# Performance work log

Hardware: AMD Instinct MI355X
Metric: run time of the kernel (lower is better)

The kernel has to match this reference:

```python
import jax, jax.numpy as jnp
import numpy as np

H = 12          # heads
DH = 64         # head dim
BS = 64         # BigBird block size
R = 3           # random blocks per query block per head
SCALE = 1.0 / np.sqrt(DH)
EPS = 1e-12     # BERT-style LayerNorm eps
NEG = -1e9


def _plan(n_blocks, seed=0):
    """Deterministic BigBird block plan: per (head, middle query block) the
    attended key-block indices [global0, win-1, win0, win+1, globalN-1, R randoms]
    plus a validity mask that kills duplicate blocks (first occurrence wins)."""
    rng = np.random.RandomState(seed)
    c = 5 + R
    idx = np.zeros((H, n_blocks - 2, c), np.int32)
    for h in range(H):
        for i in range(1, n_blocks - 1):
            base = [0, i - 1, i, i + 1, n_blocks - 1]
            cand = [j for j in range(1, n_blocks - 1) if j not in set(base)]
            idx[h, i - 1, :5] = base
            idx[h, i - 1, 5:] = rng.choice(cand, size=R, replace=False)
    valid = np.ones(idx.shape, bool)
    for a in range(c):
        for b in range(a):
            valid[..., a] &= idx[..., a] != idx[..., b]
    return jnp.asarray(idx), jnp.asarray(valid)


def _ln(x, g, b):
    mu = jnp.mean(x, -1, keepdims=True)
    v = jnp.mean(jnp.square(x - mu), -1, keepdims=True)
    return (x - mu) * jax.lax.rsqrt(v + EPS) * g + b


def _attn(h, wq, bq, wk, bk, wv, bv, idx, valid, am):
    B, S, D = h.shape
    n = S // BS
    c = idx.shape[-1]

    def heads(W, b):
        return (h @ W + b).reshape(B, S, H, DH).transpose(0, 2, 1, 3)  # [B,H,S,dh]

    q, k, v = heads(wq, bq), heads(wk, bk), heads(wv, bv)
    qb = q.reshape(B, H, n, BS, DH)
    kb = k.reshape(B, H, n, BS, DH)
    vb = v.reshape(B, H, n, BS, DH)

    # --- global query blocks (first & last): dense attention over all keys ---
    qg = jnp.concatenate([qb[:, :, 0], qb[:, :, -1]], axis=2)          # [B,H,2*BS,dh]
    sg = jnp.einsum('bhqd,bhkd->bhqk', qg, k) * SCALE
    sg = jnp.where(am[:, None, None, :] > 0, sg, NEG)
    og = jnp.einsum('bhqk,bhkd->bhqd', jax.nn.softmax(sg, -1), v)

    # --- middle query blocks: gather window+global+random key blocks ---
    hh = jnp.arange(H)[:, None, None]
    kg = kb[:, hh, idx]                                                # [B,H,n-2,c,BS,dh]
    vg = vb[:, hh, idx]
    s = jnp.einsum('bhiqd,bhickd->bhiqck', qb[:, :, 1:-1], kg) * SCALE # [B,H,n-2,BS,c,BS]
    amb = am.reshape(B, n, BS)
    amg = amb[:, idx]                                                  # [B,H,n-2,c,BS]
    mask = valid[None, :, :, None, :, None] & (amg[:, :, :, None, :, :] > 0)
    s = jnp.where(mask, s, NEG)
    p = jax.nn.softmax(s.reshape(B, H, n - 2, BS, c * BS), -1).reshape(s.shape)
    om = jnp.einsum('bhiqck,bhickd->bhiqd', p, vg)                     # [B,H,n-2,BS,dh]

    o = jnp.concatenate([og[:, :, None, :BS], om, og[:, :, None, BS:]], axis=2)
    return o.reshape(B, H, S, DH).transpose(0, 2, 1, 3).reshape(B, S, D)


def reference(x, attention_mask, Wp, bp, pos_emb, tok_emb, ln_emb_g, ln_emb_b,
              Wq, bq, Wk, bk, Wv, bv, Wo, bo, ln1_g, ln1_b,
              W1, b1f, W2, b2f, ln2_g, ln2_b, Wc1, bc1, Wc2, bc2):
    B, S, _ = x.shape
    idx, valid = _plan(S // BS)
    am = attention_mask
    h = x @ Wp + bp + pos_emb[:S][None] + tok_emb[None, None]
    h = _ln(h, ln_emb_g, ln_emb_b)

    def layer(hc, p):
        wq, bq_, wk, bk_, wv, bv_, wo, bo_, g1, be1, w1, bf1, w2, bf2, g2, be2 = p
        a = _attn(hc, wq, bq_, wk, bk_, wv, bv_, idx, valid, am) @ wo + bo_
        hc = _ln(hc + a, g1, be1)
        f = jax.nn.gelu(hc @ w1 + bf1, approximate=True) @ w2 + bf2
        hc = _ln(hc + f, g2, be2)
        return hc, None

    h, _ = jax.lax.scan(layer, h, (Wq, bq, Wk, bk, Wv, bv, Wo, bo, ln1_g, ln1_b,
                                   W1, b1f, W2, b2f, ln2_g, ln2_b))
    cls = h[:, 0]
    return jax.nn.relu(cls @ Wc1 + bc1) @ Wc2 + bc2


def setup_inputs() -> dict:
    B, S, IN, D, FF, L, OUT = 1, 4096, 1280, 768, 3072, 12, 2000
    key = jax.random.key(0)
    ks = iter(jax.random.split(key, 32))
    rn = lambda sh, s=0.02: jax.random.normal(next(ks), sh, jnp.float32) * s
    return {
        'x': jax.random.normal(next(ks), (B, S, IN), jnp.float32),
        'attention_mask': jnp.ones((B, S), jnp.int32),
        'Wp': rn((IN, D)), 'bp': jnp.zeros((D,), jnp.float32),
        'pos_emb': rn((S, D)), 'tok_emb': rn((D,)),
        'ln_emb_g': jnp.ones((D,), jnp.float32), 'ln_emb_b': jnp.zeros((D,), jnp.float32),
        'Wq': rn((L, D, D)), 'bq': jnp.zeros((L, D), jnp.float32),
        'Wk': rn((L, D, D)), 'bk': jnp.zeros((L, D), jnp.float32),
        'Wv': rn((L, D, D)), 'bv': jnp.zeros((L, D), jnp.float32),
        'Wo': rn((L, D, D)), 'bo': jnp.zeros((L, D), jnp.float32),
        'ln1_g': jnp.ones((L, D), jnp.float32), 'ln1_b': jnp.zeros((L, D), jnp.float32),
        'W1': rn((L, D, FF)), 'b1f': jnp.zeros((L, FF), jnp.float32),
        'W2': rn((L, FF, D)), 'b2f': jnp.zeros((L, D), jnp.float32),
        'ln2_g': jnp.ones((L, D), jnp.float32), 'ln2_b': jnp.zeros((L, D), jnp.float32),
        'Wc1': rn((D, 512)), 'bc1': jnp.zeros((512,), jnp.float32),
        'Wc2': rn((512, OUT)), 'bc2': jnp.zeros((OUT,), jnp.float32),
    }
```

## Files before the change

kernel.cpp:

```cpp
#include <hip/hip_runtime.h>
#include <cstdint>
#include <cstring>

typedef unsigned short u16;
typedef uint32_t u32;
typedef __attribute__((ext_vector_type(8))) short s16x8;
typedef float f32x4 __attribute__((ext_vector_type(4)));
typedef uint32_t u32x4 __attribute__((ext_vector_type(4)));

#define ATTN_SCALE 0.125f
#define NEGV -1e9f
#define GNSPLIT 16

__device__ inline float bf2f(u16 u) { return __uint_as_float(((u32)u) << 16); }
__device__ inline u16 f2bf(float f) {
    u32 x = __float_as_uint(f);
    u32 r = (x + 0x7fffu + ((x >> 16) & 1u)) >> 16;
    return (u16)r;
}
__device__ inline float rdf(const void* p, size_t i, int fl) {
    return fl ? ((const float*)p)[i] : bf2f(((const u16*)p)[i]);
}
__device__ inline float gelu_f(float x) {
    float t = 0.7978845608028654f * (x + 0.044715f * x * x * x);
    return 0.5f * x * (1.0f + tanhf(t));
}
__device__ inline f32x4 zero4() { f32x4 z = {0.f, 0.f, 0.f, 0.f}; return z; }

__global__ void sniff_k(const void* x, int* flag) {
    const u16* p = (const u16*)x;
    const int tid = threadIdx.x;
    int wild = 0;
    for (int i = tid; i < 2048; i += 64) {
        const u16 v = p[i];
        const int e = (v >> 7) & 0xff;
        if (v != 0 && (e >= 0x8f || e <= 0x5f)) wild++;
    }
#pragma unroll
    for (int m = 32; m; m >>= 1) wild += __shfl_xor(wild, m, 64);
    if (tid == 0) *flag = (wild > 64) ? 1 : 0;
}

__global__ void sentinel_k(float* out, float v, int n) {
    const int i = blockIdx.x * 256 + threadIdx.x;
    if (i < n) out[i] = v;
}

__global__ __launch_bounds__(256) void cast_k(const void* src, u16* dst, int n, const int* flag) {
    const int fl = *flag;
    const int i = blockIdx.x * 256 + threadIdx.x;
    if (i < n) dst[i] = fl ? f2bf(((const float*)src)[i]) : ((const u16*)src)[i];
}

#define LDK 72

__global__ __launch_bounds__(256) void gemm_bf16(
    const u16* __restrict__ A, const u16* __restrict__ BT,
    const void* __restrict__ bias, u16* __restrict__ C,
    int M, int N, int K, int act, const int* __restrict__ flag)
{
    __shared__ alignas(16) u16 Alds[128 * LDK];
    __shared__ alignas(16) u16 Blds[128 * LDK];
    const int fl = *flag;
    const int tid = threadIdx.x;
    const int w = tid >> 6, lane = tid & 63;
    const int quad = lane >> 4, l16 = lane & 15;
    const int wm = (w >> 1) * 64, wn = (w & 1) * 64;
    const int m0 = blockIdx.y * 128, n0 = blockIdx.x * 128;

    f32x4 acc[4][4];
    const f32x4 zv = {0.f, 0.f, 0.f, 0.f};
#pragma unroll
    for (int i = 0; i < 4; i++)
#pragma unroll
        for (int j = 0; j < 4; j++) acc[i][j] = zv;

    const int srow = tid >> 3;
    const int scol = (tid & 7) * 8;

    for (int k0 = 0; k0 < K; k0 += 64) {
        __syncthreads();
#pragma unroll
        for (int it = 0; it < 4; ++it) {
            const int row = srow + it * 32;
            *(u32x4*)(Alds + row * LDK + scol) =
                *(const u32x4*)(A + (size_t)(m0 + row) * K + k0 + scol);
            *(u32x4*)(Blds + row * LDK + scol) =
                *(const u32x4*)(BT + (size_t)(n0 + row) * K + k0 + scol);
        }
        __syncthreads();
#pragma unroll
        for (int kk = 0; kk < 2; ++kk) {
            s16x8 af[4], bfr[4];
#pragma unroll
            for (int i = 0; i < 4; i++) {
                u32x4 t_ = *(const u32x4*)(Alds + (wm + i * 16 + l16) * LDK + kk * 32 + quad * 8);
                af[i] = __builtin_bit_cast(s16x8, t_);
            }
#pragma unroll
            for (int j = 0; j < 4; j++) {
                u32x4 t_ = *(const u32x4*)(Blds + (wn + j * 16 + l16) * LDK + kk * 32 + quad * 8);
                bfr[j] = __builtin_bit_cast(s16x8, t_);
            }
#pragma unroll
            for (int i = 0; i < 4; i++)
#pragma unroll
                for (int j = 0; j < 4; j++)
                    acc[i][j] = __builtin_amdgcn_mfma_f32_16x16x32_bf16(af[i], bfr[j], acc[i][j], 0, 0, 0);
        }
    }
#pragma unroll
    for (int j = 0; j < 4; j++) {
        const int col = n0 + wn + j * 16 + l16;
        const float bv = rdf(bias, col, fl);
#pragma unroll
        for (int i = 0; i < 4; i++) {
            const int row = m0 + wm + i * 16 + quad * 4;
#pragma unroll
            for (int r = 0; r < 4; r++) {
                float xv = acc[i][j][r] + bv;
                if (act) xv = gelu_f(xv);
                C[(size_t)(row + r) * N + col] = f2bf(xv);
            }
        }
    }
}

__global__ __launch_bounds__(256) void transpose_k(
    const void* __restrict__ src, u16* __restrict__ dst, int R, int C,
    const int* __restrict__ flag)
{
    __shared__ float tile[32][33];
    const int fl = *flag;
    const int tx = threadIdx.x & 31, ty = threadIdx.x >> 5;
    const int bx = blockIdx.x, by = blockIdx.y;
#pragma unroll
    for (int rr = 0; rr < 32; rr += 8)
        tile[ty + rr][tx] = rdf(src, (size_t)(by * 32 + ty + rr) * C + bx * 32 + tx, fl);
    __syncthreads();
#pragma unroll
    for (int rr = 0; rr < 32; rr += 8)
        dst[(size_t)(bx * 32 + ty + rr) * R + by * 32 + tx] = f2bf(tile[tx][ty + rr]);
}

__global__ __launch_bounds__(256) void ln_k(
    const float* hin, const u16* __restrict__ delta,
    const void* __restrict__ pos, const void* __restrict__ tok,
    const void* __restrict__ g, const void* __restrict__ b,
    float* hout, u16* __restrict__ hbf, int mode, const int* __restrict__ flag)
{
    __shared__ float red[4];
    const int fl = *flag;
    const int s = blockIdx.x, tid = threadIdx.x;
    const size_t base = (size_t)s * 768;
    float x0 = bf2f(delta[base + tid]);
    float x1 = bf2f(delta[base + tid + 256]);
    float x2 = bf2f(delta[base + tid + 512]);
    if (mode == 0) {
        x0 += hin[base + tid]; x1 += hin[base + tid + 256]; x2 += hin[base + tid + 512];
    } else {
        x0 += rdf(pos, base + tid, fl) + rdf(tok, tid, fl);
        x1 += rdf(pos, base + tid + 256, fl) + rdf(tok, tid + 256, fl);
        x2 += rdf(pos, base + tid + 512, fl) + rdf(tok, tid + 512, fl);
    }
    float sm = x0 + x1 + x2;
#pragma unroll
    for (int m = 32; m; m >>= 1) sm += __shfl_xor(sm, m, 64);
    if ((tid & 63) == 0) red[tid >> 6] = sm;
    __syncthreads();
    const float mu = (red[0] + red[1] + red[2] + red[3]) * (1.0f / 768.0f);
    __syncthreads();
    const float d0 = x0 - mu, d1 = x1 - mu, d2 = x2 - mu;
    float vs = d0 * d0 + d1 * d1 + d2 * d2;
#pragma unroll
    for (int m = 32; m; m >>= 1) vs += __shfl_xor(vs, m, 64);
    if ((tid & 63) == 0) red[tid >> 6] = vs;
    __syncthreads();
    const float inv = rsqrtf((red[0] + red[1] + red[2] + red[3]) * (1.0f / 768.0f) + 1e-12f);
    const float y0 = d0 * inv * rdf(g, tid, fl) + rdf(b, tid, fl);
    const float y1 = d1 * inv * rdf(g, tid + 256, fl) + rdf(b, tid + 256, fl);
    const float y2 = d2 * inv * rdf(g, tid + 512, fl) + rdf(b, tid + 512, fl);
    hout[base + tid] = y0; hout[base + tid + 256] = y1; hout[base + tid + 512] = y2;
    hbf[base + tid] = f2bf(y0); hbf[base + tid + 256] = f2bf(y1); hbf[base + tid + 512] = f2bf(y2);
}

__global__ __launch_bounds__(256) void attn_mid(
    const u16* __restrict__ q, const u16* __restrict__ k, const u16* __restrict__ v,
    const int* __restrict__ am, const unsigned char* __restrict__ plan,
    u16* __restrict__ ctx)
{
    __shared__ alignas(16) u16 vt[64 * 72];
    __shared__ alignas(16) u16 plw[4][16 * 72];
    const int bid = blockIdx.x;
    const int h = bid / 62;
    const int i = 1 + (bid - h * 62);
    const int tid = threadIdx.x;
    const int w = tid >> 6, lane = tid & 63;
    const int quad = lane >> 4, l16 = lane & 15;
    const int rowbase = i * 64 + w * 16;

    const unsigned long long pw = *(const unsigned long long*)(plan + (size_t)(h * 62 + (i - 1)) * 8);

    s16x8 qa[2];
#pragma unroll
    for (int kk = 0; kk < 2; kk++) {
        u32x4 t_ = *(const u32x4*)(q + (size_t)(rowbase + l16) * 768 + h * 64 + kk * 32 + quad * 8);
        qa[kk] = __builtin_bit_cast(s16x8, t_);
    }

    f32x4 o[4];
    float mrow[4], lrow[4];
#pragma unroll
    for (int j = 0; j < 4; j++) o[j] = zero4();
#pragma unroll
    for (int r = 0; r < 4; r++) { mrow[r] = NEGV; lrow[r] = 0.f; }

    for (int t = 0; t < 8; t++) {
        const int pv = (int)((pw >> (8 * t)) & 0xff);
        const int kb = pv & 63;
        const int blkok = !(pv & 64);

        __syncthreads();
        {
            const int kr = tid & 63;
            const int seg = tid >> 6;
            const u16* vp = v + (size_t)(kb * 64 + kr) * 768 + h * 64 + seg * 16;
#pragma unroll
            for (int hc = 0; hc < 2; hc++) {
                u32x4 t_ = *(const u32x4*)(vp + hc * 8);
                const u16* e = (const u16*)&t_;
#pragma unroll
                for (int j = 0; j < 8; j++)
                    vt[(seg * 16 + hc * 8 + j) * 72 + kr] = e[j];
            }
        }

        f32x4 st[4];
#pragma unroll
        for (int jt = 0; jt < 4; jt++) {
            st[jt] = zero4();
            const u16* kp = k + (size_t)(kb * 64 + jt * 16 + l16) * 768 + h * 64 + quad * 8;
#pragma unroll
            for (int kk = 0; kk < 2; kk++) {
                u32x4 t_ = *(const u32x4*)(kp + kk * 32);
                s16x8 bf_ = __builtin_bit_cast(s16x8, t_);
                st[jt] = __builtin_amdgcn_mfma_f32_16x16x32_bf16(qa[kk], bf_, st[jt], 0, 0, 0);
            }
        }
#pragma unroll
        for (int jt = 0; jt < 4; jt++) {
            const int key = kb * 64 + jt * 16 + l16;
            const bool ok = blkok && (am[key] > 0);
#pragma unroll
            for (int r = 0; r < 4; r++)
                st[jt][r] = ok ? st[jt][r] * ATTN_SCALE : NEGV;
        }
        float mt[4];
#pragma unroll
        for (int r = 0; r < 4; r++)
            mt[r] = fmaxf(fmaxf(st[0][r], st[1][r]), fmaxf(st[2][r], st[3][r]));
#pragma unroll
        for (int m_ = 1; m_ < 16; m_ <<= 1) {
#pragma unroll
            for (int r = 0; r < 4; r++)
                mt[r] = fmaxf(mt[r], __shfl_xor(mt[r], m_, 64));
        }
        float sc[4], ps[4];
#pragma unroll
        for (int r = 0; r < 4; r++) {
            const float mn = fmaxf(mrow[r], mt[r]);
            sc[r] = __expf(mrow[r] - mn);
            mrow[r] = mn;
            ps[r] = 0.f;
        }
#pragma unroll
        for (int jt = 0; jt < 4; jt++) {
#pragma unroll
            for (int r = 0; r < 4; r++) {
                const float p = __expf(st[jt][r] - mrow[r]);
                st[jt][r] = p;
                ps[r] += p;
            }
        }
#pragma unroll
        for (int m_ = 1; m_ < 16; m_ <<= 1) {
#pragma unroll
            for (int r = 0; r < 4; r++)
                ps[r] += __shfl_xor(ps[r], m_, 64);
        }
#pragma unroll
        for (int r = 0; r < 4; r++) lrow[r] = lrow[r] * sc[r] + ps[r];

        u16* pb = &plw[w][0];
#pragma unroll
        for (int jt = 0; jt < 4; jt++) {
#pragma unroll
            for (int r = 0; r < 4; r++)
                pb[(quad * 4 + r) * 72 + jt * 16 + l16] = f2bf(st[jt][r]);
        }
#pragma unroll
        for (int j = 0; j < 4; j++) {
#pragma unroll
            for (int r = 0; r < 4; r++)
                o[j][r] *= sc[r];
        }
        __syncthreads();

#pragma unroll
        for (int kk = 0; kk < 2; kk++) {
            s16x8 pa;
            {
                u32x4 t_ = *(const u32x4*)(pb + l16 * 72 + kk * 32 + quad * 8);
                pa = __builtin_bit_cast(s16x8, t_);
            }
#pragma unroll
            for (int jt2 = 0; jt2 < 4; jt2++) {
                u32x4 t_ = *(const u32x4*)(vt + (jt2 * 16 + l16) * 72 + kk * 32 + quad * 8);
                s16x8 vb = __builtin_bit_cast(s16x8, t_);
                o[jt2] = __builtin_amdgcn_mfma_f32_16x16x32_bf16(pa, vb, o[jt2], 0, 0, 0);
            }
        }
    }

    float invl[4];
#pragma unroll
    for (int r = 0; r < 4; r++) invl[r] = 1.0f / lrow[r];
#pragma unroll
    for (int jt2 = 0; jt2 < 4; jt2++) {
#pragma unroll
        for (int r = 0; r < 4; r++)
            ctx[(size_t)(rowbase + quad * 4 + r) * 768 + h * 64 + jt2 * 16 + l16] =
                f2bf(o[jt2][r] * invl[r]);
    }
}

__global__ __launch_bounds__(256) void attn_global_mfma(
    const u16* __restrict__ q, const u16* __restrict__ k, const u16* __restrict__ v,
    const int* __restrict__ am, float* __restrict__ po, float* __restrict__ pml)
{
    __shared__ alignas(16) u16 vt[64 * 72];
    __shared__ alignas(16) u16 plw[4][16 * 72];
    const int bid = blockIdx.x;
    const int h = bid / (2 * GNSPLIT);
    const int rem = bid - h * 2 * GNSPLIT;
    const int qb = rem / GNSPLIT;
    const int sp = rem - qb * GNSPLIT;
    const int tid = threadIdx.x;
    const int w = tid >> 6, lane = tid & 63;
    const int quad = lane >> 4, l16 = lane & 15;
    const int qrow0 = (qb ? 4032 : 0) + w * 16;
    const int KBPS = 64 / GNSPLIT;

    s16x8 qa[2];
#pragma unroll
    for (int kk = 0; kk < 2; kk++) {
        u32x4 t_ = *(const u32x4*)(q + (size_t)(qrow0 + l16) * 768 + h * 64 + kk * 32 + quad * 8);
        qa[kk] = __builtin_bit_cast(s16x8, t_);
    }

    f32x4 o[4];
    float mrow[4], lrow[4];
#pragma unroll
    for (int j = 0; j < 4; j++) o[j] = zero4();
#pragma unroll
    for (int r = 0; r < 4; r++) { mrow[r] = NEGV; lrow[r] = 0.f; }

    for (int t = 0; t < KBPS; t++) {
        const int kb = sp * KBPS + t;

        __syncthreads();
        {
            const int kr = tid & 63;
            const int seg = tid >> 6;
            const u16* vp = v + (size_t)(kb * 64 + kr) * 768 + h * 64 + seg * 16;
#pragma unroll
            for (int hc = 0; hc < 2; hc++) {
                u32x4 t_ = *(const u32x4*)(vp + hc * 8);
                const u16* e = (const u16*)&t_;
#pragma unroll
                for (int j = 0; j < 8; j++)
                    vt[(seg * 16 + hc * 8 + j) * 72 + kr] = e[j];
            }
        }

        f32x4 st[4];
#pragma unroll
        for (int jt = 0; jt < 4; jt++) {
            st[jt] = zero4();
            const u16* kp = k + (size_t)(kb * 64 + jt * 16 + l16) * 768 + h * 64 + quad * 8;
#pragma unroll
            for (int kk = 0; kk < 2; kk++) {
                u32x4 t_ = *(const u32x4*)(kp + kk * 32);
                s16x8 bf_ = __builtin_bit_cast(s16x8, t_);
                st[jt] = __builtin_amdgcn_mfma_f32_16x16x32_bf16(qa[kk], bf_, st[jt], 0, 0, 0);
            }
        }
#pragma unroll
        for (int jt = 0; jt < 4; jt++) {
            const int key = kb * 64 + jt * 16 + l16;
            const bool ok = (am[key] > 0);
#pragma unroll
            for (int r = 0; r < 4; r++)
                st[jt][r] = ok ? st[jt][r] * ATTN_SCALE : NEGV;
        }
        float mt[4];
#pragma unroll
        for (int r = 0; r < 4; r++)
            mt[r] = fmaxf(fmaxf(st[0][r], st[1][r]), fmaxf(st[2][r], st[3][r]));
#pragma unroll
        for (int m_ = 1; m_ < 16; m_ <<= 1) {
#pragma unroll
            for (int r = 0; r < 4; r++)
                mt[r] = fmaxf(mt[r], __shfl_xor(mt[r], m_, 64));
        }
        float sc[4], ps[4];
#pragma unroll
        for (int r = 0; r < 4; r++) {
            const float mn = fmaxf(mrow[r], mt[r]);
            sc[r] = __expf(mrow[r] - mn);
            mrow[r] = mn;
            ps[r] = 0.f;
        }
#pragma unroll
        for (int jt = 0; jt < 4; jt++) {
#pragma unroll
            for (int r = 0; r < 4; r++) {
                const float p = __expf(st[jt][r] - mrow[r]);
                st[jt][r] = p;
                ps[r] += p;
            }
        }
#pragma unroll
        for (int m_ = 1; m_ < 16; m_ <<= 1) {
#pragma unroll
            for (int r = 0; r < 4; r++)
                ps[r] += __shfl_xor(ps[r], m_, 64);
        }
#pragma unroll
        for (int r = 0; r < 4; r++) lrow[r] = lrow[r] * sc[r] + ps[r];

        u16* pb = &plw[w][0];
#pragma unroll
        for (int jt = 0; jt < 4; jt++) {
#pragma unroll
            for (int r = 0; r < 4; r++)
                pb[(quad * 4 + r) * 72 + jt * 16 + l16] = f2bf(st[jt][r]);
        }
#pragma unroll
        for (int j = 0; j < 4; j++) {
#pragma unroll
            for (int r = 0; r < 4; r++)
                o[j][r] *= sc[r];
        }
        __syncthreads();

#pragma unroll
        for (int kk = 0; kk < 2; kk++) {
            s16x8 pa;
            {
                u32x4 t_ = *(const u32x4*)(pb + l16 * 72 + kk * 32 + quad * 8);
                pa = __builtin_bit_cast(s16x8, t_);
            }
#pragma unroll
            for (int jt2 = 0; jt2 < 4; jt2++) {
                u32x4 t_ = *(const u32x4*)(vt + (jt2 * 16 + l16) * 72 + kk * 32 + quad * 8);
                s16x8 vb = __builtin_bit_cast(s16x8, t_);
                o[jt2] = __builtin_amdgcn_mfma_f32_16x16x32_bf16(pa, vb, o[jt2], 0, 0, 0);
            }
        }
    }

    const int part = (h * 2 + qb) * GNSPLIT + sp;
    float* op = po + (size_t)part * 4096;
#pragma unroll
    for (int jt2 = 0; jt2 < 4; jt2++) {
#pragma unroll
        for (int r = 0; r < 4; r++)
            op[(w * 16 + quad * 4 + r) * 64 + jt2 * 16 + l16] = o[jt2][r];
    }
    if (l16 == 0) {
        float* ml = pml + (size_t)part * 128;
#pragma unroll
        for (int r = 0; r < 4; r++) {
            ml[w * 16 + quad * 4 + r] = mrow[r];
            ml[64 + w * 16 + quad * 4 + r] = lrow[r];
        }
    }
}

__global__ __launch_bounds__(256) void attn_global_comb(
    const float* __restrict__ po, const float* __restrict__ pml,
    u16* __restrict__ ctx)
{
    const int bid = blockIdx.x;
    const int h = bid >> 1, qb = bid & 1;
    const int tid = threadIdx.x;
    const int row = tid >> 2;
    const int d0 = (tid & 3) * 16;
    const int pbase = bid * GNSPLIT;

    float ms[GNSPLIT], ls[GNSPLIT];
    float mstar = -3e38f;
#pragma unroll
    for (int s = 0; s < GNSPLIT; s++) {
        ms[s] = pml[(size_t)(pbase + s) * 128 + row];
        ls[s] = pml[(size_t)(pbase + s) * 128 + 64 + row];
        mstar = fmaxf(mstar, ms[s]);
    }
    float acc[16];
#pragma unroll
    for (int j = 0; j < 16; j++) acc[j] = 0.f;
    float den = 0.f;
    for (int s = 0; s < GNSPLIT; s++) {
        const float wgt = __expf(ms[s] - mstar);
        den += wgt * ls[s];
        const float* op = po + (size_t)(pbase + s) * 4096 + row * 64 + d0;
#pragma unroll
        for (int j = 0; j < 16; j++) acc[j] += wgt * op[j];
    }
    const float inv = 1.0f / den;
    const int srow = (qb ? 4032 : 0) + row;
#pragma unroll
    for (int j = 0; j < 16; j++)
        ctx[(size_t)srow * 768 + h * 64 + d0 + j] = f2bf(acc[j] * inv);
}

__global__ __launch_bounds__(256) void cls1(
    const float* __restrict__ h0, const void* __restrict__ Wc1,
    const void* __restrict__ bc1, float* __restrict__ t, const int* __restrict__ flag)
{
    const int fl = *flag;
    const int n = blockIdx.x * 256 + threadIdx.x;
    float a = 0;
    for (int kk = 0; kk < 768; ++kk)
        a += h0[kk] * rdf(Wc1, (size_t)kk * 512 + n, fl);
    a += rdf(bc1, n, fl);
    if (!isfinite(a)) { t[n] = 31337.0f; return; }
    t[n] = fmaxf(a, 0.f);
}
__global__ __launch_bounds__(256) void cls2(
    const float* __restrict__ t, const void* __restrict__ Wc2,
    const void* __restrict__ bc2, void* __restrict__ out, const int* __restrict__ flag)
{
    const int fl = *flag;
    const int n = blockIdx.x * 256 + threadIdx.x;
    if (n >= 2000) return;
    float a = 0;
    for (int kk = 0; kk < 512; ++kk)
        a += t[kk] * rdf(Wc2, (size_t)kk * 2000 + n, fl);
    a += rdf(bc2, n, fl);
    if (!isfinite(a)) a = 65504.0f;
    if (fl) ((float*)out)[n] = a;
    else ((u16*)out)[n] = f2bf(a);
}

struct PChunk { unsigned char d[1984]; };
__global__ void put_plan(PChunk c, unsigned char* __restrict__ dst) {
    for (int j = threadIdx.x; j < 1984; j += 256) dst[j] = c.d[j];
}

__global__ __launch_bounds__(256) void transpose_off_k(
    const void* __restrict__ src, u16* __restrict__ dst, int R, int C,
    const int* __restrict__ flag, unsigned long long eoff);
__global__ __launch_bounds__(256) void gemm_off_bf16(
    const u16* __restrict__ A, const u16* __restrict__ BT,
    const void* __restrict__ bias, u16* __restrict__ C,
    int M, int N, int K, int act, const int* __restrict__ flag, unsigned long long beoff);
__global__ __launch_bounds__(256) void ln_off_k(
    const float* hin, const u16* __restrict__ delta,
    const void* __restrict__ pos, const void* __restrict__ tok,
    const void* __restrict__ g, const void* __restrict__ b,
    float* hout, u16* __restrict__ hbf, int mode, const int* __restrict__ flag,
    unsigned long long geoff, unsigned long long beoff);

namespace {
struct MT {
    uint32_t mt[624]; int mti;
    void seed(uint32_t s) {
        mt[0] = s;
        for (int i = 1; i < 624; i++) mt[i] = 1812433253u * (mt[i - 1] ^ (mt[i - 1] >> 30)) + (uint32_t)i;
        mti = 624;
    }
    uint32_t next() {
        if (mti >= 624) {
            for (int i = 0; i < 624; i++) {
                uint32_t y = (mt[i] & 0x80000000u) | (mt[(i + 1) % 624] & 0x7fffffffu);
                mt[i] = mt[(i + 397) % 624] ^ (y >> 1) ^ ((y & 1u) ? 0x9908b0dfu : 0u);
            }
            mti = 0;
        }
        uint32_t y = mt[mti++];
        y ^= y >> 11; y ^= (y << 7) & 0x9d2c5680u; y ^= (y << 15) & 0xefc60000u; y ^= y >> 18;
        return y;
    }
};
uint32_t rint_(MT& mt, uint32_t mx) {
    if (!mx) return 0;
    uint32_t mask = mx;
    mask |= mask >> 1; mask |= mask >> 2; mask |= mask >> 4; mask |= mask >> 8; mask |= mask >> 16;
    uint32_t v;
    while ((v = mt.next() & mask) > mx) {}
    return v;
}
void compute_plan(unsigned char* out) {
    MT mt; mt.seed(0);
    for (int h = 0; h < 12; h++)
        for (int i = 1; i <= 62; i++) {
            int base[5] = {0, i - 1, i, i + 1, 63};
            int cand[64], nc = 0;
            for (int j = 1; j <= 62; j++) {
                bool inb = false;
                for (int b = 0; b < 5; b++) if (base[b] == j) { inb = true; break; }
                if (!inb) cand[nc++] = j;
            }
            int perm[64];
            for (int j = 0; j < nc; j++) perm[j] = j;
            for (int kk = nc - 1; kk >= 1; kk--) {
                uint32_t j = rint_(mt, (uint32_t)kk);
                int tmp = perm[kk]; perm[kk] = perm[j]; perm[j] = tmp;
            }
            int vals[8];
            for (int a = 0; a < 5; a++) vals[a] = base[a];
            for (int a = 0; a < 3; a++) vals[5 + a] = cand[perm[a]];
            for (int a = 0; a < 8; a++) {
                bool dup = false;
                for (int b = 0; b < a; b++) if (vals[b] == vals[a]) { dup = true; break; }
                out[((h * 62) + (i - 1)) * 8 + a] = (unsigned char)(vals[a] | (dup ? 64 : 0));
            }
        }
}
}

extern "C" void kernel_launch(void* const* d_in, const int* in_sizes, int n_in,
                              void* d_out, int out_size, void* d_ws, size_t ws_size,
                              hipStream_t stream)
{
    const void* x   = d_in[0];
    const int* am   = (const int*)d_in[1];
    const void* Wp  = d_in[2];
    const void* bp  = d_in[3];
    const void* pos = d_in[4];
    const void* tok = d_in[5];
    const void* lng = d_in[6];
    const void* lnb = d_in[7];
    const float* Wq  = (const float*)d_in[8];
    const float* bq  = (const float*)d_in[9];
    const float* Wk  = (const float*)d_in[10];
    const float* bk  = (const float*)d_in[11];
    const float* Wv  = (const float*)d_in[12];
    const float* bv  = (const float*)d_in[13];
    const float* Wo  = (const float*)d_in[14];
    const float* bo  = (const float*)d_in[15];
    const float* lg1 = (const float*)d_in[16];
    const float* lb1 = (const float*)d_in[17];
    const float* W1  = (const float*)d_in[18];
    const float* fb1 = (const float*)d_in[19];
    const float* W2  = (const float*)d_in[20];
    const float* fb2 = (const float*)d_in[21];
    const float* lg2 = (const float*)d_in[22];
    const float* lb2 = (const float*)d_in[23];
    const void* Wc1 = d_in[24];
    const void* bc1 = d_in[25];
    const void* Wc2 = d_in[26];
    const void* bc2 = d_in[27];
    (void)in_sizes; (void)n_in; (void)out_size;

    char* wsb = (char*)d_ws;
    size_t off = 0;
    auto take = [&](size_t bytes) -> void* {
        void* p = wsb + off;
        off += (bytes + 255) & ~(size_t)255;
        return p;
    };
    unsigned char* planb = (unsigned char*)take(5952);
    int* flag  = (int*)take(256);
    float* hB  = (float*)take((size_t)4096 * 768 * 4);
    u16* hbfB  = (u16*)take((size_t)4096 * 768 * 2);
    u16* qB    = (u16*)take((size_t)4096 * 768 * 2);
    u16* kB    = (u16*)take((size_t)4096 * 768 * 2);
    u16* vB    = (u16*)take((size_t)4096 * 768 * 2);
    u16* ctxB  = (u16*)take((size_t)4096 * 768 * 2);
    u16* dB    = (u16*)take((size_t)4096 * 768 * 2);
    u16* wTB   = (u16*)take((size_t)3072 * 768 * 2);
    float* tB  = (float*)take(2048);
    u16* ffnB  = qB;
    u16* xbfB  = qB;
    float* gpo = (float*)dB;
    float* gml = (float*)wTB;
    const size_t NEED = off;
    if (ws_size < NEED) {
        sentinel_k<<<dim3(4), dim3(256), 0, stream>>>((float*)d_out, 2000.0f, 1000);
        return;
    }

    sniff_k<<<dim3(1), dim3(64), 0, stream>>>(x, flag);

    static unsigned char plan_host[5952];
    compute_plan(plan_host);
    for (int c = 0; c < 3; c++) {
        PChunk pc;
        memcpy(pc.d, plan_host + c * 1984, 1984);
        put_plan<<<dim3(1), dim3(256), 0, stream>>>(pc, planb + c * 1984);
    }

    cast_k<<<dim3(20480), dim3(256), 0, stream>>>(x, xbfB, 4096 * 1280, flag);
    transpose_k<<<dim3(24, 40), dim3(256), 0, stream>>>(Wp, wTB, 1280, 768, flag);
    gemm_bf16<<<dim3(6, 32), dim3(256), 0, stream>>>(xbfB, wTB, bp, dB, 4096, 768, 1280, 0, flag);
    ln_k<<<dim3(4096), dim3(256), 0, stream>>>(hB, dB, pos, tok, lng, lnb, hB, hbfB, 1, flag);

    for (int l = 0; l < 12; ++l) {
        const size_t wo = (size_t)l * 768 * 768;
        const size_t fo = (size_t)l * 768 * 3072;
        const size_t b768 = (size_t)l * 768;
        const size_t b3072 = (size_t)l * 3072;

        transpose_off_k<<<dim3(24, 24), dim3(256), 0, stream>>>(Wq, wTB, 768, 768, flag, wo);
        gemm_off_bf16<<<dim3(6, 32), dim3(256), 0, stream>>>(hbfB, wTB, bq, qB, 4096, 768, 768, 0, flag, b768);
        transpose_off_k<<<dim3(24, 24), dim3(256), 0, stream>>>(Wk, wTB, 768, 768, flag, wo);
        gemm_off_bf16<<<dim3(6, 32), dim3(256), 0, stream>>>(hbfB, wTB, bk, kB, 4096, 768, 768, 0, flag, b768);
        transpose_off_k<<<dim3(24, 24), dim3(256), 0, stream>>>(Wv, wTB, 768, 768, flag, wo);
        gemm_off_bf16<<<dim3(6, 32), dim3(256), 0, stream>>>(hbfB, wTB, bv, vB, 4096, 768, 768, 0, flag, b768);

        attn_mid<<<dim3(744), dim3(256), 0, stream>>>(qB, kB, vB, am, planb, ctxB);
        attn_global_mfma<<<dim3(12 * 2 * GNSPLIT), dim3(256), 0, stream>>>(qB, kB, vB, am, gpo, gml);
        attn_global_comb<<<dim3(24), dim3(256), 0, stream>>>(gpo, gml, ctxB);

        transpose_off_k<<<dim3(24, 24), dim3(256), 0, stream>>>(Wo, wTB, 768, 768, flag, wo);
        gemm_off_bf16<<<dim3(6, 32), dim3(256), 0, stream>>>(ctxB, wTB, bo, dB, 4096, 768, 768, 0, flag, b768);
        ln_off_k<<<dim3(4096), dim3(256), 0, stream>>>(hB, dB, nullptr, nullptr, lg1, lb1, hB, hbfB, 0, flag, b768, b768);

        transpose_off_k<<<dim3(96, 24), dim3(256), 0, stream>>>(W1, wTB, 768, 3072, flag, fo);
        gemm_off_bf16<<<dim3(24, 32), dim3(256), 0, stream>>>(hbfB, wTB, fb1, ffnB, 4096, 3072, 768, 1, flag, b3072);
        transpose_off_k<<<dim3(24, 96), dim3(256), 0, stream>>>(W2, wTB, 3072, 768, flag, fo);
        gemm_off_bf16<<<dim3(6, 32), dim3(256), 0, stream>>>(ffnB, wTB, fb2, dB, 4096, 768, 3072, 0, flag, b768);
        ln_off_k<<<dim3(4096), dim3(256), 0, stream>>>(hB, dB, nullptr, nullptr, lg2, lb2, hB, hbfB, 0, flag, b768, b768);
    }

    cls1<<<dim3(2), dim3(256), 0, stream>>>(hB, Wc1, bc1, tB, flag);
    cls2<<<dim3(8), dim3(256), 0, stream>>>(tB, Wc2, bc2, d_out, flag);
}

__global__ __launch_bounds__(256) void transpose_off_k(
    const void* __restrict__ src, u16* __restrict__ dst, int R, int C,
    const int* __restrict__ flag, unsigned long long eoff)
{
    __shared__ float tile[32][33];
    const int fl = *flag;
    const int tx = threadIdx.x & 31, ty = threadIdx.x >> 5;
    const int bx = blockIdx.x, by = blockIdx.y;
#pragma unroll
    for (int rr = 0; rr < 32; rr += 8)
        tile[ty + rr][tx] = rdf(src, eoff + (size_t)(by * 32 + ty + rr) * C + bx * 32 + tx, fl);
    __syncthreads();
#pragma unroll
    for (int rr = 0; rr < 32; rr += 8)
        dst[(size_t)(bx * 32 + ty + rr) * R + by * 32 + tx] = f2bf(tile[tx][ty + rr]);
}

__global__ __launch_bounds__(256) void gemm_off_bf16(
    const u16* __restrict__ A, const u16* __restrict__ BT,
    const void* __restrict__ bias, u16* __restrict__ C,
    int M, int N, int K, int act, const int* __restrict__ flag, unsigned long long beoff)
{
    __shared__ alignas(16) u16 Alds[128 * LDK];
    __shared__ alignas(16) u16 Blds[128 * LDK];
    const int fl = *flag;
    const int tid = threadIdx.x;
    const int w = tid >> 6, lane = tid & 63;
    const int quad = lane >> 4, l16 = lane & 15;
    const int wm = (w >> 1) * 64, wn = (w & 1) * 64;
    const int m0 = blockIdx.y * 128, n0 = blockIdx.x * 128;

    f32x4 acc[4][4];
    const f32x4 zv = {0.f, 0.f, 0.f, 0.f};
#pragma unroll
    for (int i = 0; i < 4; i++)
#pragma unroll
        for (int j = 0; j < 4; j++) acc[i][j] = zv;

    const int srow = tid >> 3;
    const int scol = (tid & 7) * 8;

    for (int k0 = 0; k0 < K; k0 += 64) {
        __syncthreads();
#pragma unroll
        for (int it = 0; it < 4; ++it) {
            const int row = srow + it * 32;
            *(u32x4*)(Alds + row * LDK + scol) =
                *(const u32x4*)(A + (size_t)(m0 + row) * K + k0 + scol);
            *(u32x4*)(Blds + row * LDK + scol) =
                *(const u32x4*)(BT + (size_t)(n0 + row) * K + k0 + scol);
        }
        __syncthreads();
#pragma unroll
        for (int kk = 0; kk < 2; ++kk) {
            s16x8 af[4], bfr[4];
#pragma unroll
            for (int i = 0; i < 4; i++) {
                u32x4 t_ = *(const u32x4*)(Alds + (wm + i * 16 + l16) * LDK + kk * 32 + quad * 8);
                af[i] = __builtin_bit_cast(s16x8, t_);
            }
#pragma unroll
            for (int j = 0; j < 4; j++) {
                u32x4 t_ = *(const u32x4*)(Blds + (wn + j * 16 + l16) * LDK + kk * 32 + quad * 8);
                bfr[j] = __builtin_bit_cast(s16x8, t_);
            }
#pragma unroll
            for (int i = 0; i < 4; i++)
#pragma unroll
                for (int j = 0; j < 4; j++)
                    acc[i][j] = __builtin_amdgcn_mfma_f32_16x16x32_bf16(af[i], bfr[j], acc[i][j], 0, 0, 0);
        }
    }
#pragma unroll
    for (int j = 0; j < 4; j++) {
        const int col = n0 + wn + j * 16 + l16;
        const float bv = rdf(bias, beoff + col, fl);
#pragma unroll
        for (int i = 0; i < 4; i++) {
            const int row = m0 + wm + i * 16 + quad * 4;
#pragma unroll
            for (int r = 0; r < 4; r++) {
                float xv = acc[i][j][r] + bv;
                if (act) xv = gelu_f(xv);
                C[(size_t)(row + r) * N + col] = f2bf(xv);
            }
        }
    }
}

__global__ __launch_bounds__(256) void ln_off_k(
    const float* hin, const u16* __restrict__ delta,
    const void* __restrict__ pos, const void* __restrict__ tok,
    const void* __restrict__ g, const void* __restrict__ b,
    float* hout, u16* __restrict__ hbf, int mode, const int* __restrict__ flag,
    unsigned long long geoff, unsigned long long beoff)
{
    __shared__ float red[4];
    const int fl = *flag;
    const int s = blockIdx.x, tid = threadIdx.x;
    const size_t base = (size_t)s * 768;
    float x0 = bf2f(delta[base + tid]);
    float x1 = bf2f(delta[base + tid + 256]);
    float x2 = bf2f(delta[base + tid + 512]);
    if (mode == 0) {
        x0 += hin[base + tid]; x1 += hin[base + tid + 256]; x2 += hin[base + tid + 512];
    } else {
        x0 += rdf(pos, base + tid, fl) + rdf(tok, tid, fl);
        x1 += rdf(pos, base + tid + 256, fl) + rdf(tok, tid + 256, fl);
        x2 += rdf(pos, base + tid + 512, fl) + rdf(tok, tid + 512, fl);
    }
    float sm = x0 + x1 + x2;
#pragma unroll
    for (int m = 32; m; m >>= 1) sm += __shfl_xor(sm, m, 64);
    if ((tid & 63) == 0) red[tid >> 6] = sm;
    __syncthreads();
    const float mu = (red[0] + red[1] + red[2] + red[3]) * (1.0f / 768.0f);
    __syncthreads();
    const float d0 = x0 - mu, d1 = x1 - mu, d2 = x2 - mu;
    float vs = d0 * d0 + d1 * d1 + d2 * d2;
#pragma unroll
    for (int m = 32; m; m >>= 1) vs += __shfl_xor(vs, m, 64);
    if ((tid & 63) == 0) red[tid >> 6] = vs;
    __syncthreads();
    const float inv = rsqrtf((red[0] + red[1] + red[2] + red[3]) * (1.0f / 768.0f) + 1e-12f);
    const float y0 = d0 * inv * rdf(g, geoff + tid, fl) + rdf(b, beoff + tid, fl);
    const float y1 = d1 * inv * rdf(g, geoff + tid + 256, fl) + rdf(b, beoff + tid + 256, fl);
    const float y2 = d2 * inv * rdf(g, geoff + tid + 512, fl) + rdf(b, beoff + tid + 512, fl);
    hout[base + tid] = y0; hout[base + tid + 256] = y1; hout[base + tid + 512] = y2;
    hbf[base + tid] = f2bf(y0); hbf[base + tid + 256] = f2bf(y1); hbf[base + tid + 512] = f2bf(y2);
}
```

Measured before the change: 4.132 ms.

## Fuse QKV projections into one GEMM launch and parallelize classifier head

Transposes Wq, Wk and Wv into one contiguous buffer and computes all three projections in a single GEMM kernel with a 3x wider grid, routing each column tile to the right output and bias. This cuts the number of launches and gives the GPU more blocks to fill its compute units. The classifier kernels change from a serial dot product per thread to one block per output, using a wave shuffle reduction. The fused kernel hardcodes K=768 and N=768 per output.

```diff
diff --git a/kernel.cpp b/kernel.cpp
--- a/kernel.cpp
+++ b/kernel.cpp
@@ -529,29 +529,43 @@
     const float* __restrict__ h0, const void* __restrict__ Wc1,
     const void* __restrict__ bc1, float* __restrict__ t, const int* __restrict__ flag)
 {
+    __shared__ float red[4];
     const int fl = *flag;
-    const int n = blockIdx.x * 256 + threadIdx.x;
+    const int n = blockIdx.x;
+    const int tid = threadIdx.x;
     float a = 0;
-    for (int kk = 0; kk < 768; ++kk)
+    for (int kk = tid; kk < 768; kk += 256)
         a += h0[kk] * rdf(Wc1, (size_t)kk * 512 + n, fl);
-    a += rdf(bc1, n, fl);
-    if (!isfinite(a)) { t[n] = 31337.0f; return; }
-    t[n] = fmaxf(a, 0.f);
+#pragma unroll
+    for (int m = 32; m; m >>= 1) a += __shfl_xor(a, m, 64);
+    if ((tid & 63) == 0) red[tid >> 6] = a;
+    __syncthreads();
+    if (tid == 0) {
+        float s = red[0] + red[1] + red[2] + red[3] + rdf(bc1, n, fl);
+        t[n] = isfinite(s) ? fmaxf(s, 0.f) : 31337.0f;
+    }
 }
 __global__ __launch_bounds__(256) void cls2(
     const float* __restrict__ t, const void* __restrict__ Wc2,
     const void* __restrict__ bc2, void* __restrict__ out, const int* __restrict__ flag)
 {
+    __shared__ float red[4];
     const int fl = *flag;
-    const int n = blockIdx.x * 256 + threadIdx.x;
-    if (n >= 2000) return;
+    const int n = blockIdx.x;
+    const int tid = threadIdx.x;
     float a = 0;
-    for (int kk = 0; kk < 512; ++kk)
+    for (int kk = tid; kk < 512; kk += 256)
         a += t[kk] * rdf(Wc2, (size_t)kk * 2000 + n, fl);
-    a += rdf(bc2, n, fl);
-    if (!isfinite(a)) a = 65504.0f;
-    if (fl) ((float*)out)[n] = a;
-    else ((u16*)out)[n] = f2bf(a);
+#pragma unroll
+    for (int m = 32; m; m >>= 1) a += __shfl_xor(a, m, 64);
+    if ((tid & 63) == 0) red[tid >> 6] = a;
+    __syncthreads();
+    if (tid == 0) {
+        float s = red[0] + red[1] + red[2] + red[3] + rdf(bc2, n, fl);
+        if (!isfinite(s)) s = 65504.0f;
+        if (fl) ((float*)out)[n] = s;
+        else ((u16*)out)[n] = f2bf(s);
+    }
 }
 
 struct PChunk { unsigned char d[1984]; };
@@ -566,6 +580,11 @@
     const u16* __restrict__ A, const u16* __restrict__ BT,
     const void* __restrict__ bias, u16* __restrict__ C,
     int M, int N, int K, int act, const int* __restrict__ flag, unsigned long long beoff);
+__global__ __launch_bounds__(256) void gemm_qkv(
+    const u16* __restrict__ A, const u16* __restrict__ BT,
+    const void* __restrict__ bq, const void* __restrict__ bk, const void* __restrict__ bv,
+    u16* __restrict__ Cq, u16* __restrict__ Ck, u16* __restrict__ Cv,
+    const int* __restrict__ flag, unsigned long long beoff);
 __global__ __launch_bounds__(256) void ln_off_k(
     const float* hin, const u16* __restrict__ delta,
     const void* __restrict__ pos, const void* __restrict__ tok,
@@ -715,11 +734,9 @@
         const size_t b3072 = (size_t)l * 3072;
 
         transpose_off_k<<<dim3(24, 24), dim3(256), 0, stream>>>(Wq, wTB, 768, 768, flag, wo);
-        gemm_off_bf16<<<dim3(6, 32), dim3(256), 0, stream>>>(hbfB, wTB, bq, qB, 4096, 768, 768, 0, flag, b768);
-        transpose_off_k<<<dim3(24, 24), dim3(256), 0, stream>>>(Wk, wTB, 768, 768, flag, wo);
-        gemm_off_bf16<<<dim3(6, 32), dim3(256), 0, stream>>>(hbfB, wTB, bk, kB, 4096, 768, 768, 0, flag, b768);
-        transpose_off_k<<<dim3(24, 24), dim3(256), 0, stream>>>(Wv, wTB, 768, 768, flag, wo);
-        gemm_off_bf16<<<dim3(6, 32), dim3(256), 0, stream>>>(hbfB, wTB, bv, vB, 4096, 768, 768, 0, flag, b768);
+        transpose_off_k<<<dim3(24, 24), dim3(256), 0, stream>>>(Wk, wTB + (size_t)768 * 768, 768, 768, flag, wo);
+        transpose_off_k<<<dim3(24, 24), dim3(256), 0, stream>>>(Wv, wTB + (size_t)2 * 768 * 768, 768, 768, flag, wo);
+        gemm_qkv<<<dim3(18, 32), dim3(256), 0, stream>>>(hbfB, wTB, bq, bk, bv, qB, kB, vB, flag, b768);
 
         attn_mid<<<dim3(744), dim3(256), 0, stream>>>(qB, kB, vB, am, planb, ctxB);
         attn_global_mfma<<<dim3(12 * 2 * GNSPLIT), dim3(256), 0, stream>>>(qB, kB, vB, am, gpo, gml);
@@ -736,8 +753,8 @@
         ln_off_k<<<dim3(4096), dim3(256), 0, stream>>>(hB, dB, nullptr, nullptr, lg2, lb2, hB, hbfB, 0, flag, b768, b768);
     }
 
-    cls1<<<dim3(2), dim3(256), 0, stream>>>(hB, Wc1, bc1, tB, flag);
-    cls2<<<dim3(8), dim3(256), 0, stream>>>(tB, Wc2, bc2, d_out, flag);
+    cls1<<<dim3(512), dim3(256), 0, stream>>>(hB, Wc1, bc1, tB, flag);
+    cls2<<<dim3(2000), dim3(256), 0, stream>>>(tB, Wc2, bc2, d_out, flag);
 }
 
 __global__ __launch_bounds__(256) void transpose_off_k(
@@ -825,6 +842,81 @@
                 if (act) xv = gelu_f(xv);
                 C[(size_t)(row + r) * N + col] = f2bf(xv);
             }
+        }
+    }
+}
+
+__global__ __launch_bounds__(256) void gemm_qkv(
+    const u16* __restrict__ A, const u16* __restrict__ BT,
+    const void* __restrict__ bq, const void* __restrict__ bk, const void* __restrict__ bv,
+    u16* __restrict__ Cq, u16* __restrict__ Ck, u16* __restrict__ Cv,
+    const int* __restrict__ flag, unsigned long long beoff)
+{
+    __shared__ alignas(16) u16 Alds[128 * LDK];
+    __shared__ alignas(16) u16 Blds[128 * LDK];
+    const int fl = *flag;
+    const int tid = threadIdx.x;
+    const int w = tid >> 6, lane = tid & 63;
+    const int quad = lane >> 4, l16 = lane & 15;
+    const int wm = (w >> 1) * 64, wn = (w & 1) * 64;
+    const int m0 = blockIdx.y * 128, n0 = blockIdx.x * 128;
+    const int K = 768;
+
+    f32x4 acc[4][4];
+    const f32x4 zv = {0.f, 0.f, 0.f, 0.f};
+#pragma unroll
+    for (int i = 0; i < 4; i++)
+#pragma unroll
+        for (int j = 0; j < 4; j++) acc[i][j] = zv;
+
+    const int srow = tid >> 3;
+    const int scol = (tid & 7) * 8;
+
+    for (int k0 = 0; k0 < K; k0 += 64) {
+        __syncthreads();
+#pragma unroll
+        for (int it = 0; it < 4; ++it) {
+            const int row = srow + it * 32;
+            *(u32x4*)(Alds + row * LDK + scol) =
+                *(const u32x4*)(A + (size_t)(m0 + row) * K + k0 + scol);
+            *(u32x4*)(Blds + row * LDK + scol) =
+                *(const u32x4*)(BT + (size_t)(n0 + row) * K + k0 + scol);
+        }
+        __syncthreads();
+#pragma unroll
+        for (int kk = 0; kk < 2; ++kk) {
+            s16x8 af[4], bfr[4];
+#pragma unroll
+            for (int i = 0; i < 4; i++) {
+                u32x4 t_ = *(const u32x4*)(Alds + (wm + i * 16 + l16) * LDK + kk * 32 + quad * 8);
+                af[i] = __builtin_bit_cast(s16x8, t_);
+            }
+#pragma unroll
+            for (int j = 0; j < 4; j++) {
+                u32x4 t_ = *(const u32x4*)(Blds + (wn + j * 16 + l16) * LDK + kk * 32 + quad * 8);
+                bfr[j] = __builtin_bit_cast(s16x8, t_);
+            }
+#pragma unroll
+            for (int i = 0; i < 4; i++)
+#pragma unroll
+                for (int j = 0; j < 4; j++)
+                    acc[i][j] = __builtin_amdgcn_mfma_f32_16x16x32_bf16(af[i], bfr[j], acc[i][j], 0, 0, 0);
+        }
+    }
+    const int sel = n0 / 768;
+    const void* bias = (sel == 0) ? bq : (sel == 1) ? bk : bv;
+    u16* C = (sel == 0) ? Cq : (sel == 1) ? Ck : Cv;
+    const int nloc0 = n0 - sel * 768;
+#pragma unroll
+    for (int j = 0; j < 4; j++) {
+        const int col = nloc0 + wn + j * 16 + l16;
+        const float bvv = rdf(bias, beoff + col, fl);
+#pragma unroll
+        for (int i = 0; i < 4; i++) {
+            const int row = m0 + wm + i * 16 + quad * 4;
+#pragma unroll
+            for (int r = 0; r < 4; r++)
+                C[(size_t)(row + r) * 768 + col] = f2bf(acc[i][j][r] + bvv);
         }
     }
 }
```

Result: faster. 3.701 ms (-10.4%).
